# Performance work log

Hardware: AMD Instinct MI355X
Metric: run time of the kernel (lower is better)

Reference implementation:

```python
import math
import jax, jax.numpy as jnp
import numpy as np

# ---- hard-coded constants from the source module ----
T_H = 1.5; M = 60; DT = T_H / M; SQDT = math.sqrt(DT)
ALPHA = 0.8; RHO = 0.3; SQ1MR2 = math.sqrt(1.0 - RHO * RHO)
GAMMA = 5.0; KAPPA_Y = 1.2; LB_W = 1e-3
R = 0.02; SIGMA = 0.2; SIGMA_Y = 0.3; THETA_Y = 0.0; PI_CAP = 2.0
RPTS = 128       # sub_batch (one accumulation iteration)
REPEATS = 128    # total repeats == sub_batch -> single loop pass
N_PTS = 32       # number of eval states
HID = 64


def setup_inputs():
    key = jax.random.key(0)
    ks = jax.random.split(key, 8)
    W = 0.8 + 0.4 * jax.random.uniform(ks[0], (N_PTS, 1), jnp.float32)   # W0_range
    Y = -1.0 + 2.0 * jax.random.uniform(ks[1], (N_PTS, 1), jnp.float32)  # Y0_range
    TmT = jnp.full((N_PTS, 1), T_H, jnp.float32)
    B = RPTS * N_PTS
    # [sim(+/-), draw(z1/z2), step, path, 1] -- fresh noise per antithetic branch, as in torch
    noise = jax.random.normal(ks[2], (2, 2, M, B, 1), jnp.float32)
    w1 = 0.1 * jax.random.normal(ks[3], (3, HID), jnp.float32)
    b1 = jnp.zeros((HID,), jnp.float32)
    w2 = 0.1 * jax.random.normal(ks[4], (HID, HID), jnp.float32)
    b2 = jnp.zeros((HID,), jnp.float32)
    w3 = 0.1 * jax.random.normal(ks[5], (HID, 1), jnp.float32)
    b3 = jnp.zeros((1,), jnp.float32)
    return {"W": W, "TmT": TmT, "Y": Y, "noise": noise,
            "w1": w1, "b1": b1, "w2": w2, "b2": b2, "w3": w3, "b3": b3}


def _policy(params, W, TmT, Y):
    w1, b1, w2, b2, w3, b3 = params
    x = jnp.concatenate([W, TmT, Y], axis=-1)          # [B,3]
    h = jnp.tanh(x @ w1 + b1)
    h = jnp.tanh(h @ w2 + b2)
    return h @ w3 + b3                                 # [B,1]


def _simulate(params, W0, Y0, z1, z2, anti):
    """60-step Euler-Maruyama; returns CRRA utility U(W_T), shape [B,1]."""
    logW = jnp.log(jnp.clip(W0, LB_W, None))
    TmT0 = jnp.full_like(W0, T_H)

    def step(carry, zs):
        logW, Y, TmT = carry
        z1s, z2s = zs
        pi = _policy(params, jnp.exp(logW), TmT, Y)
        zW = anti * z1s
        zY = anti * (RHO * z1s + SQ1MR2 * z2s)
        drift = R + pi * (SIGMA * ALPHA * Y)
        var = (pi * SIGMA) ** 2
        logW = logW + (drift - 0.5 * var) * DT + pi * SIGMA * SQDT * zW
        Y = Y + KAPPA_Y * (THETA_Y - Y) * DT + SIGMA_Y * SQDT * zY
        logW = jnp.log(jnp.clip(jnp.exp(logW), LB_W, None))
        return (logW, Y, TmT - DT), None

    (logW, _, _), _ = jax.lax.scan(step, (logW, Y0, TmT0), (z1, z2))
    W_T = jnp.exp(logW)
    return W_T ** (1.0 - GAMMA) / (1.0 - GAMMA)        # gamma != 1


def reference(W, TmT, Y, noise, w1, b1, w2, b2, w3, b3):
    params = (w1, b1, w2, b2, w3, b3)
    n = W.shape[0]
    Wd = jax.lax.stop_gradient(W)   # forward detaches W, Y
    Yd = jax.lax.stop_gradient(Y)
    W0 = jnp.tile(Wd, (RPTS, 1))    # [B,1]
    Y0 = jnp.tile(Yd, (RPTS, 1))
    z1p, z2p = noise[0, 0], noise[0, 1]
    z1m, z2m = noise[1, 0], noise[1, 1]

    def f(W0_, Y0_):
        U = 0.5 * (_simulate(params, W0_, Y0_, z1p, z2p, 1.0)
                   + _simulate(params, W0_, Y0_, z1m, z2m, -1.0))
        # U_avg.sum() as in torch: mean over rpts, sum over eval points
        return jnp.sum(jnp.mean(U.reshape(RPTS, n), axis=0))

    lam_full = jax.grad(f, 0)(W0, Y0)                  # [B,1]

    def g(W0_, Y0_):
        # lam.view(rpts,n,1).mean(0).sum() == sum(lam_full)/rpts
        return jnp.sum(jax.grad(f, 0)(W0_, Y0_)) / RPTS

    dW_full, dY_full = jax.grad(g, (0, 1))(W0, Y0)     # [B,1] each

    inv = 1.0 / REPEATS   # faithful to source accumulation scaling
    lam = lam_full.reshape(RPTS, n, 1).mean(0) * inv
    dlamW = dW_full.reshape(RPTS, n, 1).mean(0) * inv
    dlamY = dY_full.reshape(RPTS, n, 1).mean(0) * inv

    # project_pmp
    mu_minus_r = SIGMA * (ALPHA * Yd)
    coeff = -1.0 / (Wd * dlamW + 1e-8)
    myo = coeff * (lam * (mu_minus_r / SIGMA ** 2))
    hedge = coeff * (SIGMA * RHO * SIGMA_Y * dlamY / SIGMA ** 2)
    return jnp.clip(myo + hedge, -PI_CAP, PI_CAP)      # [n,1]
```

## Files before the change

kernel.cpp:

```cpp
#include <hip/hip_runtime.h>
#include <math.h>

#define HID    64
#define MSTEPS 60
#define NPTS   32
#define RPTSC  128
#define BTOT   (RPTSC*NPTS)
#define NSIM   (2*BTOT)
#define NWAVE  (NSIM/2)

#define C_DT     0.025f
#define C_SQDT   0.15811388300841897f
#define C_ALPHA  0.8f
#define C_RHO    0.3f
#define C_SQ1MR2 0.9539392014169456f
#define C_KAPPA  1.2f
#define C_R      0.02f
#define C_SIGMA  0.2f
#define C_SIGY   0.3f
#define C_LBW    1e-3f
#define C_LOGLBW -6.907755279f
#define C_2L2E   2.8853900817779268f

#define WAVE_LDS 3584
#define A_ROW    144
#define OFF_DV   2304
#define OFF_DA   3328

typedef _Float16 half8 __attribute__((ext_vector_type(8)));
typedef float    f32x4 __attribute__((ext_vector_type(4)));
typedef _Float16 h2    __attribute__((ext_vector_type(2)));

__device__ __forceinline__ float rlanef(float v, int l) {
    return __int_as_float(__builtin_amdgcn_readlane(__float_as_int(v), l));
}
template <int OFF>
__device__ __forceinline__ float swz(float v) {
    return __int_as_float(__builtin_amdgcn_ds_swizzle(__float_as_int(v), OFF));
}
__device__ __forceinline__ f32x4 MFMA(half8 a, half8 b, f32x4 c) {
    return __builtin_amdgcn_mfma_f32_16x16x32_f16(a, b, c, 0, 0, 0);
}
__device__ __forceinline__ int pk16(float a, float b) {
    return __builtin_bit_cast(int, __builtin_amdgcn_cvt_pkrtz(a, b));
}
__device__ __forceinline__ h2 pk2(float a, float b) {
    return __builtin_bit_cast(h2, __builtin_amdgcn_cvt_pkrtz(a, b));
}
__device__ __forceinline__ h2 permh(unsigned s0, unsigned s1, unsigned sel) {
    return __builtin_bit_cast(h2, __builtin_amdgcn_perm(s0, s1, sel));
}
__device__ __forceinline__ float tanh_fast(float xs) {
    return 1.0f - 2.0f * __builtin_amdgcn_rcpf(__builtin_amdgcn_exp2f(xs) + 1.0f);
}

__global__ __launch_bounds__(256, 4) void sim_kernel(
    const float* __restrict__ noise,
    const float* __restrict__ w1, const float* __restrict__ b1,
    const float* __restrict__ w2, const float* __restrict__ b2,
    const float* __restrict__ w3, const float* __restrict__ b3,
    const float* __restrict__ Wp, const float* __restrict__ Yp,
    float* __restrict__ sd)
{
    __shared__ __align__(16) char smem[4 * WAVE_LDS];
    const int lane = threadIdx.x & 63;
    const int quad = lane >> 4;
    const int mrow = lane & 15;
    const int par  = lane >> 5;
    char* wb = smem + (threadIdx.x >> 6) * WAVE_LDS;

    const int w = __builtin_amdgcn_readfirstlane(
        (int)((blockIdx.x * blockDim.x + threadIdx.x) >> 6));
    const int simb = w >> 11;
    const int pg   = 2*(w & 2047) + par;
    const int i    = pg & (NPTS - 1);

    const float cW  = w1[lane];
    const float cT  = w1[HID + lane];
    const float cYw = w1[2*HID + lane];
    const float b1k = b1[lane];
    const float b2k = b2[lane];
    const float b3v = b3[0];
    const float cW_s  = cW  * C_2L2E;
    const float cT_s  = cT  * C_2L2E;
    const float cYw_s = cYw * C_2L2E;
    const float b1_s  = b1k * C_2L2E;
    const float b2_s  = b2k * C_2L2E;
    const h2 cWh  = pk2(cW, cW);
    const h2 cYwh = pk2(cYw, cYw);
    const h2 cW2m = pk2(-2.0f*cW*cW,  -2.0f*cW*cW);
    const h2 cWYm = pk2(-2.0f*cW*cYw, -2.0f*cW*cYw);
    const h2 hone = {(_Float16)1.0f,  (_Float16)1.0f};
    const h2 m2h  = {(_Float16)-2.0f, (_Float16)-2.0f};

    half8 B00, B01, B02, B03, B10, B11, B12, B13, W30, W31;
    {
        half8 h;
        #define LOADB(dst, q, t) \
            { for (int j = 0; j < 8; ++j) \
                h[j] = (_Float16)w2[((q)*32 + quad*8 + j)*HID + (t)*16 + mrow]; \
              dst = h; }
        LOADB(B00, 0, 0) LOADB(B01, 0, 1) LOADB(B02, 0, 2) LOADB(B03, 0, 3)
        LOADB(B10, 1, 0) LOADB(B11, 1, 1) LOADB(B12, 1, 2) LOADB(B13, 1, 3)
        #undef LOADB
        for (int j = 0; j < 8; ++j) h[j] = (_Float16)w3[0*32 + quad*8 + j];
        W30 = h;
        for (int j = 0; j < 8; ++j) h[j] = (_Float16)w3[1*32 + quad*8 + j];
        W31 = h;
    }

    for (int off = lane*4; off < 16*A_ROW; off += 256)
        *(float*)(wb + off) = 0.0f;

    _Float16* swp = (_Float16*)(wb + lane*2);
    char* arp0 = wb + mrow*A_ROW + quad*16;

    const float* zp1 = noise + (size_t)(simb*2 + 0) * MSTEPS * BTOT + pg;
    const float* zp2 = noise + (size_t)(simb*2 + 1) * MSTEPS * BTOT + pg;

    const float anti = simb ? -1.0f : 1.0f;
    const float ksa  = C_SIGMA * C_ALPHA;
    const float ks2  = C_SIGMA * C_SIGMA;
    const float ksn  = anti * C_SIGMA * C_SQDT;
    const float kFy  = ksa * C_DT;
    const float ksd  = ks2 * C_DT;
    const float kv   = 0.5f * ks2 * C_DT;
    const float kRdt = C_R * C_DT;
    const float ky1  = anti * C_SIGY * C_SQDT * C_RHO;
    const float ky2  = anti * C_SIGY * C_SQDT * C_SQ1MR2;
    const float cYfac = 1.0f - C_KAPPA * C_DT;

    const float W0 = Wp[i];
    float L   = __logf(fmaxf(W0, C_LBW));
    float W   = __expf(L);
    float Yv  = Yp[i];
    float tmt = 1.5f;
    float gW  = 1.0f / W0;
    float hWW = -gW * gW;
    float gY  = 0.0f, hWY = 0.0f;
    float cYt = 1.0f;

    #pragma unroll 1
    for (int m = 0; m < MSTEPS; ++m) {
        asm volatile("" : "+v"(B00), "+v"(B01), "+v"(B02), "+v"(B03),
                          "+v"(B10), "+v"(B11), "+v"(B12), "+v"(B13),
                          "+v"(W30), "+v"(W31));

        const float z1 = zp1[(size_t)m * BTOT];
        const float z2 = zp2[(size_t)m * BTOT];

        const float Wb0 = rlanef(W, 0),  Wb1 = rlanef(W, 32);
        const float Yb0 = rlanef(Yv, 0), Yb1 = rlanef(Yv, 32);

        const float base1s = fmaf(tmt, cT_s, b1_s);
        {
            const float t10 = tanh_fast(fmaf(Wb0, cW_s, fmaf(Yb0, cYw_s, base1s)));
            const float t11 = tanh_fast(fmaf(Wb1, cW_s, fmaf(Yb1, cYw_s, base1s)));
            const h2 tp  = pk2(t10, t11);
            const h2 dpp = hone - tp * tp;
            const h2 ddq = tp * dpp;
            const h2 r1 = dpp * cWh;
            const h2 r2 = dpp * cYwh;
            const h2 r3 = ddq * cW2m;
            const h2 r4 = ddq * cWYm;
            swp[0*72] = tp.x;  swp[8*72]  = tp.y;
            swp[1*72] = r1.x;  swp[9*72]  = r1.y;
            swp[2*72] = r2.x;  swp[10*72] = r2.y;
            swp[3*72] = r3.x;  swp[11*72] = r3.y;
            swp[4*72] = r4.x;  swp[12*72] = r4.y;
        }

        half8 af0 = __builtin_bit_cast(half8, *(const f32x4*)arp0);
        half8 af1 = __builtin_bit_cast(half8, *(const f32x4*)(arp0 + 64));

        f32x4 acc[4];
        const f32x4 zz = {0.f, 0.f, 0.f, 0.f};
        acc[0] = MFMA(af1, B10, MFMA(af0, B00, zz));
        acc[1] = MFMA(af1, B11, MFMA(af0, B01, zz));
        acc[2] = MFMA(af1, B12, MFMA(af0, B02, zz));
        acc[3] = MFMA(af1, B13, MFMA(af0, B03, zz));

        {
            const int p = quad >> 1;
            if (!(quad & 1)) {
                #pragma unroll
                for (int t = 0; t < 4; ++t) {
                    int2 v;
                    v.x = pk16(acc[t].x, acc[t].y);
                    v.y = pk16(acc[t].z, acc[t].w);
                    *(int2*)(wb + OFF_DV + ((t*16 + mrow) << 4) + (p << 3)) = v;
                }
            } else {
                #pragma unroll
                for (int t = 0; t < 4; ++t)
                    *(_Float16*)(wb + OFF_DA + ((t*16 + mrow) << 2) + (p << 1)) =
                        (_Float16)acc[t].x;
            }
        }

        const f32x4 dvv = *(const f32x4*)(wb + OFF_DV + lane*16);
        const h2 awyp   = *(const h2*)(wb + OFF_DA + lane*4);
        {
            const unsigned q0 = __builtin_bit_cast(unsigned, dvv.x);
            const unsigned q1 = __builtin_bit_cast(unsigned, dvv.y);
            const unsigned q2 = __builtin_bit_cast(unsigned, dvv.z);
            const unsigned q3 = __builtin_bit_cast(unsigned, dvv.w);
            const h2 a0p  = permh(q2, q0, 0x05040100);
            const h2 aWp  = permh(q2, q0, 0x07060302);
            const h2 aYp  = permh(q3, q1, 0x05040100);
            const h2 aWWp = permh(q3, q1, 0x07060302);

            const float t20 = tanh_fast(fmaf((float)a0p.x, C_2L2E, b2_s));
            const float t21 = tanh_fast(fmaf((float)a0p.y, C_2L2E, b2_s));
            const h2 t2p = pk2(t20, t21);
            const h2 d2p = hone - t2p * t2p;
            const h2 qp  = (m2h * (t2p * d2p)) * aWp;
            const h2 s1 = d2p * aWp;
            const h2 s2 = d2p * aYp;
            const h2 s3 = qp * aWp + d2p * aWWp;
            const h2 s4 = qp * aYp + d2p * awyp;
            swp[0*72] = t2p.x; swp[8*72]  = t2p.y;
            swp[1*72] = s1.x;  swp[9*72]  = s1.y;
            swp[2*72] = s2.x;  swp[10*72] = s2.y;
            swp[3*72] = s3.x;  swp[11*72] = s3.y;
            swp[4*72] = s4.x;  swp[12*72] = s4.y;
        }

        half8 bf0 = __builtin_bit_cast(half8, *(const f32x4*)arp0);
        half8 bf1 = __builtin_bit_cast(half8, *(const f32x4*)(arp0 + 64));
        f32x4 acc4 = MFMA(bf1, W31, MFMA(bf0, W30, zz));

        const float pi  = swz<0x0000>(acc4.x) + b3v;
        const float pW  = swz<0x0000>(acc4.y);
        const float pY  = swz<0x0000>(acc4.z);
        const float pWW = swz<0x0000>(acc4.w);
        const float pWY = swz<0x0200>(acc4.x);

        const float Sn    = ksn * z1;
        const float say   = ksa * Yv;
        const float G     = fmaf(-ks2, pi, say);
        const float GdtSn = fmaf(G, C_DT, Sn);

        const float w2v  = W * W;
        const float piL  = pW * W;
        const float piLL = fmaf(pWW, w2v, piL);
        const float piY  = pY;
        const float piLY = pWY * W;

        const float pi2  = pi * pi;
        const float Lnew = fmaf(pi, fmaf(say, C_DT, Sn),
                                fmaf(-kv, pi2, L + kRdt));

        const float F_L  = fmaf(piL, GdtSn, 1.0f);
        const float F_Y  = fmaf(piY, GdtSn, kFy * pi);
        const float piL2 = piL * piL;
        const float F_LL = fmaf(piLL, GdtSn, -(ksd * piL2));
        const float F_LY = fmaf(piLY, GdtSn, piL * fmaf(-ksd, piY, kFy));

        const float gW2  = gW * gW;
        const float hWWn = fmaf(F_LL, gW2, F_L * hWW);
        const float hWYn = fmaf(F_LL, gW * gY,
                                fmaf(F_LY, gW * cYt, F_L * hWY));
        const float gWn  = F_L * gW;
        const float gYn  = fmaf(F_Y, cYt, F_L * gY);

        Yv  = fmaf(ky2, z2, fmaf(ky1, z1, cYfac * Yv));
        cYt *= cYfac;

        const float We   = __expf(Lnew);
        const bool  clip = (We < C_LBW);
        L   = clip ? C_LOGLBW : Lnew;
        W   = clip ? C_LBW    : We;
        gW  = clip ? 0.0f : gWn;
        gY  = clip ? 0.0f : gYn;
        hWW = clip ? 0.0f : hWWn;
        hWY = clip ? 0.0f : hWYn;
        tmt -= C_DT;
    }

    const float E   = __expf(-4.0f * L);
    const float d1  = E * gW;
    const float d2v = fmaf(-4.0f * E, gW * gW, E * hWW);
    const float d3v = fmaf(-4.0f * E, gW * gY, E * hWY);

    if ((lane & 31) == 0) {
        const int branch = simb * BTOT + pg;
        sd[         branch] = 0.5f * d1;
        sd[  NSIM + branch] = 0.5f * d2v;
        sd[2*NSIM + branch] = 0.5f * d3v;
    }
}

__global__ __launch_bounds__(512) void proj_kernel(
    const float* __restrict__ sd,
    const float* __restrict__ Wp,
    const float* __restrict__ Yp,
    float* __restrict__ out)
{
    __shared__ float red[3 * 512];
    const int tid = threadIdx.x;
    const int i = tid & 31;
    const int c = tid >> 5;
    float lam = 0.f, dW = 0.f, dY = 0.f;
    #pragma unroll 4
    for (int jj = 0; jj < 16; ++jj) {
        const int idx = i + ((jj*16 + c) << 5);
        lam += sd[idx];
        dW  += sd[NSIM + idx];
        dY  += sd[2*NSIM + idx];
    }
    red[tid] = lam; red[512 + tid] = dW; red[1024 + tid] = dY;
    __syncthreads();
    if (tid < NPTS) {
        float l = 0.f, w = 0.f, y = 0.f;
        #pragma unroll
        for (int c2 = 0; c2 < 16; ++c2) {
            l += red[c2*32 + i];
            w += red[512 + c2*32 + i];
            y += red[1024 + c2*32 + i];
        }
        l *= (1.0f / 2097152.0f);
        w *= (1.0f / 268435456.0f);
        y *= (1.0f / 268435456.0f);
        const float Wv = Wp[i], Yv = Yp[i];
        const float mmr   = C_SIGMA * (C_ALPHA * Yv);
        const float sig2  = C_SIGMA * C_SIGMA;
        const float coeff = -1.0f / (Wv * w + 1e-8f);
        const float myo   = coeff * (l * (mmr / sig2));
        const float hedge = coeff * (C_SIGMA * C_RHO * C_SIGY * y / sig2);
        float v = myo + hedge;
        v = fminf(fmaxf(v, -2.0f), 2.0f);
        out[i] = v;
    }
}

extern "C" void kernel_launch(void* const* d_in, const int* in_sizes, int n_in,
                              void* d_out, int out_size, void* d_ws, size_t ws_size,
                              hipStream_t stream) {
    const float* Wp    = (const float*)d_in[0];
    const float* Yp    = (const float*)d_in[2];
    const float* noise = (const float*)d_in[3];
    const float* w1    = (const float*)d_in[4];
    const float* b1    = (const float*)d_in[5];
    const float* w2    = (const float*)d_in[6];
    const float* b2    = (const float*)d_in[7];
    const float* w3    = (const float*)d_in[8];
    const float* b3    = (const float*)d_in[9];
    float* out = (float*)d_out;
    float* sd  = (float*)d_ws;

    hipLaunchKernelGGL(sim_kernel, dim3(NWAVE/4), dim3(256), 0, stream,
                       noise, w1, b1, w2, b2, w3, b3, Wp, Yp, sd);
    hipLaunchKernelGGL(proj_kernel, dim3(1), dim3(512), 0, stream, sd, Wp, Yp, out);
}
```

Baseline: 163.0 us.

## Replace second LDS round trip and output MFMA with in-register layer-2 epilogue and DPP reduction

New measurement: 171.1 us. 5.0% more time.

```diff
diff --git a/kernel.cpp b/kernel.cpp
--- a/kernel.cpp
+++ b/kernel.cpp
@@ -22,10 +22,8 @@
 #define C_LOGLBW -6.907755279f
 #define C_2L2E   2.8853900817779268f
 
-#define WAVE_LDS 3584
+#define WAVE_LDS 2304
 #define A_ROW    144
-#define OFF_DV   2304
-#define OFF_DA   3328
 
 typedef _Float16 half8 __attribute__((ext_vector_type(8)));
 typedef float    f32x4 __attribute__((ext_vector_type(4)));
@@ -41,17 +39,23 @@
 __device__ __forceinline__ f32x4 MFMA(half8 a, half8 b, f32x4 c) {
     return __builtin_amdgcn_mfma_f32_16x16x32_f16(a, b, c, 0, 0, 0);
 }
-__device__ __forceinline__ int pk16(float a, float b) {
-    return __builtin_bit_cast(int, __builtin_amdgcn_cvt_pkrtz(a, b));
-}
 __device__ __forceinline__ h2 pk2(float a, float b) {
     return __builtin_bit_cast(h2, __builtin_amdgcn_cvt_pkrtz(a, b));
 }
-__device__ __forceinline__ h2 permh(unsigned s0, unsigned s1, unsigned sel) {
-    return __builtin_bit_cast(h2, __builtin_amdgcn_perm(s0, s1, sel));
-}
 __device__ __forceinline__ float tanh_fast(float xs) {
     return 1.0f - 2.0f * __builtin_amdgcn_rcpf(__builtin_amdgcn_exp2f(xs) + 1.0f);
+}
+template <int CTRL>
+__device__ __forceinline__ float dppadd(float v) {
+    return v + __int_as_float(__builtin_amdgcn_update_dpp(
+        0, __float_as_int(v), CTRL, 0xf, 0xf, false));
+}
+__device__ __forceinline__ float red64(float v) {
+    v = dppadd<0x121>(v);
+    v = dppadd<0x122>(v);
+    v = dppadd<0x124>(v);
+    v = dppadd<0x128>(v);
+    return v + swz<0x401F>(v);
 }
 
 __global__ __launch_bounds__(256, 4) void sim_kernel(
@@ -91,9 +95,13 @@
     const h2 cW2m = pk2(-2.0f*cW*cW,  -2.0f*cW*cW);
     const h2 cWYm = pk2(-2.0f*cW*cYw, -2.0f*cW*cYw);
     const h2 hone = {(_Float16)1.0f,  (_Float16)1.0f};
-    const h2 m2h  = {(_Float16)-2.0f, (_Float16)-2.0f};
-
-    half8 B00, B01, B02, B03, B10, B11, B12, B13, W30, W31;
+
+    const float w3q0 = (quad & 1) ? 0.0f : w3[ 0 + mrow];
+    const float w3q1 = (quad & 1) ? 0.0f : w3[16 + mrow];
+    const float w3q2 = (quad & 1) ? 0.0f : w3[32 + mrow];
+    const float w3q3 = (quad & 1) ? 0.0f : w3[48 + mrow];
+
+    half8 B00, B01, B02, B03, B10, B11, B12, B13;
     {
         half8 h;
         #define LOADB(dst, q, t) \
@@ -103,10 +111,6 @@
         LOADB(B00, 0, 0) LOADB(B01, 0, 1) LOADB(B02, 0, 2) LOADB(B03, 0, 3)
         LOADB(B10, 1, 0) LOADB(B11, 1, 1) LOADB(B12, 1, 2) LOADB(B13, 1, 3)
         #undef LOADB
-        for (int j = 0; j < 8; ++j) h[j] = (_Float16)w3[0*32 + quad*8 + j];
-        W30 = h;
-        for (int j = 0; j < 8; ++j) h[j] = (_Float16)w3[1*32 + quad*8 + j];
-        W31 = h;
     }
 
     for (int off = lane*4; off < 16*A_ROW; off += 256)
@@ -140,14 +144,18 @@
     float gY  = 0.0f, hWY = 0.0f;
     float cYt = 1.0f;
 
+    float z1c = zp1[0];
+    float z2c = zp2[0];
+
     #pragma unroll 1
     for (int m = 0; m < MSTEPS; ++m) {
         asm volatile("" : "+v"(B00), "+v"(B01), "+v"(B02), "+v"(B03),
-                          "+v"(B10), "+v"(B11), "+v"(B12), "+v"(B13),
-                          "+v"(W30), "+v"(W31));
-
-        const float z1 = zp1[(size_t)m * BTOT];
-        const float z2 = zp2[(size_t)m * BTOT];
+                          "+v"(B10), "+v"(B11), "+v"(B12), "+v"(B13));
+
+        const float z1 = z1c, z2 = z2c;
+        const int mn = (m + 1 < MSTEPS) ? m + 1 : m;
+        z1c = zp1[(size_t)mn * BTOT];
+        z2c = zp2[(size_t)mn * BTOT];
 
         const float Wb0 = rlanef(W, 0),  Wb1 = rlanef(W, 32);
         const float Yb0 = rlanef(Yv, 0), Yb1 = rlanef(Yv, 32);
@@ -180,61 +188,40 @@
         acc[2] = MFMA(af1, B12, MFMA(af0, B02, zz));
         acc[3] = MFMA(af1, B13, MFMA(af0, B03, zz));
 
-        {
-            const int p = quad >> 1;
-            if (!(quad & 1)) {
-                #pragma unroll
-                for (int t = 0; t < 4; ++t) {
-                    int2 v;
-                    v.x = pk16(acc[t].x, acc[t].y);
-                    v.y = pk16(acc[t].z, acc[t].w);
-                    *(int2*)(wb + OFF_DV + ((t*16 + mrow) << 4) + (p << 3)) = v;
-                }
-            } else {
-                #pragma unroll
-                for (int t = 0; t < 4; ++t)
-                    *(_Float16*)(wb + OFF_DA + ((t*16 + mrow) << 2) + (p << 1)) =
-                        (_Float16)acc[t].x;
-            }
+        float awy[4];
+        awy[0] = swz<0x401F>(acc[0].x);
+        awy[1] = swz<0x401F>(acc[1].x);
+        awy[2] = swz<0x401F>(acc[2].x);
+        awy[3] = swz<0x401F>(acc[3].x);
+        const float w3qa[4] = {w3q0, w3q1, w3q2, w3q3};
+
+        float p0 = 0.f, p1 = 0.f, p2 = 0.f, p3 = 0.f, p4 = 0.f;
+        #pragma unroll
+        for (int t = 0; t < 4; ++t) {
+            const float a0  = acc[t].x, aW = acc[t].y;
+            const float aY  = acc[t].z, aWW = acc[t].w;
+            const float aWY = awy[t];
+            const float t2  = tanh_fast(fmaf(a0, C_2L2E, b2_s));
+            const float d2  = fmaf(-t2, t2, 1.0f);
+            const float td  = t2 * d2;
+            const float q   = -2.0f * (td * aW);
+            const float s1  = d2 * aW;
+            const float s2  = d2 * aY;
+            const float s3  = fmaf(q, aW, d2 * aWW);
+            const float s4  = fmaf(q, aY, d2 * aWY);
+            const float w3t = w3qa[t];
+            p0 = fmaf(t2, w3t, p0);
+            p1 = fmaf(s1, w3t, p1);
+            p2 = fmaf(s2, w3t, p2);
+            p3 = fmaf(s3, w3t, p3);
+            p4 = fmaf(s4, w3t, p4);
         }
 
-        const f32x4 dvv = *(const f32x4*)(wb + OFF_DV + lane*16);
-        const h2 awyp   = *(const h2*)(wb + OFF_DA + lane*4);
-        {
-            const unsigned q0 = __builtin_bit_cast(unsigned, dvv.x);
-            const unsigned q1 = __builtin_bit_cast(unsigned, dvv.y);
-            const unsigned q2 = __builtin_bit_cast(unsigned, dvv.z);
-            const unsigned q3 = __builtin_bit_cast(unsigned, dvv.w);
-            const h2 a0p  = permh(q2, q0, 0x05040100);
-            const h2 aWp  = permh(q2, q0, 0x07060302);
-            const h2 aYp  = permh(q3, q1, 0x05040100);
-            const h2 aWWp = permh(q3, q1, 0x07060302);
-
-            const float t20 = tanh_fast(fmaf((float)a0p.x, C_2L2E, b2_s));
-            const float t21 = tanh_fast(fmaf((float)a0p.y, C_2L2E, b2_s));
-            const h2 t2p = pk2(t20, t21);
-            const h2 d2p = hone - t2p * t2p;
-            const h2 qp  = (m2h * (t2p * d2p)) * aWp;
-            const h2 s1 = d2p * aWp;
-            const h2 s2 = d2p * aYp;
-            const h2 s3 = qp * aWp + d2p * aWWp;
-            const h2 s4 = qp * aYp + d2p * awyp;
-            swp[0*72] = t2p.x; swp[8*72]  = t2p.y;
-            swp[1*72] = s1.x;  swp[9*72]  = s1.y;
-            swp[2*72] = s2.x;  swp[10*72] = s2.y;
-            swp[3*72] = s3.x;  swp[11*72] = s3.y;
-            swp[4*72] = s4.x;  swp[12*72] = s4.y;
-        }
-
-        half8 bf0 = __builtin_bit_cast(half8, *(const f32x4*)arp0);
-        half8 bf1 = __builtin_bit_cast(half8, *(const f32x4*)(arp0 + 64));
-        f32x4 acc4 = MFMA(bf1, W31, MFMA(bf0, W30, zz));
-
-        const float pi  = swz<0x0000>(acc4.x) + b3v;
-        const float pW  = swz<0x0000>(acc4.y);
-        const float pY  = swz<0x0000>(acc4.z);
-        const float pWW = swz<0x0000>(acc4.w);
-        const float pWY = swz<0x0200>(acc4.x);
+        const float pi  = red64(p0) + b3v;
+        const float pW  = red64(p1);
+        const float pY  = red64(p2);
+        const float pWW = red64(p3);
+        const float pWY = red64(p4);
 
         const float Sn    = ksn * z1;
         const float say   = ksa * Yv;
```

## Interleave two independent path pairs per wave to hide MFMA and LDS latency

Applied to the files above, without the earlier changes.

Measured after the change: 171.8 us. 5.4% more time.

```diff
diff --git a/kernel.cpp b/kernel.cpp
--- a/kernel.cpp
+++ b/kernel.cpp
@@ -7,7 +7,8 @@
 #define RPTSC  128
 #define BTOT   (RPTSC*NPTS)
 #define NSIM   (2*BTOT)
-#define NWAVE  (NSIM/2)
+#define NWAVE  2048
+#define NBLK   (NWAVE/4)
 
 #define C_DT     0.025f
 #define C_SQDT   0.15811388300841897f
@@ -22,7 +23,7 @@
 #define C_LOGLBW -6.907755279f
 #define C_2L2E   2.8853900817779268f
 
-#define WAVE_LDS 3584
+#define PAIR_LDS 3584
 #define A_ROW    144
 #define OFF_DV   2304
 #define OFF_DA   3328
@@ -54,7 +55,77 @@
     return 1.0f - 2.0f * __builtin_amdgcn_rcpf(__builtin_amdgcn_exp2f(xs) + 1.0f);
 }
 
-__global__ __launch_bounds__(256, 4) void sim_kernel(
+__device__ __forceinline__ void l1_jets(
+    _Float16* swp, float bW0, float bW1, float bY0, float bY1,
+    float base1s, float cW_s, float cYw_s,
+    h2 cWh, h2 cYwh, h2 cW2m, h2 cWYm)
+{
+    const h2 hone = {(_Float16)1.0f, (_Float16)1.0f};
+    const float t10 = tanh_fast(fmaf(bW0, cW_s, fmaf(bY0, cYw_s, base1s)));
+    const float t11 = tanh_fast(fmaf(bW1, cW_s, fmaf(bY1, cYw_s, base1s)));
+    const h2 tp  = pk2(t10, t11);
+    const h2 dpp = hone - tp * tp;
+    const h2 ddq = tp * dpp;
+    const h2 r1 = dpp * cWh;
+    const h2 r2 = dpp * cYwh;
+    const h2 r3 = ddq * cW2m;
+    const h2 r4 = ddq * cWYm;
+    swp[0*72] = tp.x;  swp[8*72]  = tp.y;
+    swp[1*72] = r1.x;  swp[9*72]  = r1.y;
+    swp[2*72] = r2.x;  swp[10*72] = r2.y;
+    swp[3*72] = r3.x;  swp[11*72] = r3.y;
+    swp[4*72] = r4.x;  swp[12*72] = r4.y;
+}
+
+__device__ __forceinline__ void dxpose(char* wb, const f32x4* acc, int quad, int mrow)
+{
+    const int p = quad >> 1;
+    if (!(quad & 1)) {
+        #pragma unroll
+        for (int t = 0; t < 4; ++t) {
+            int2 v;
+            v.x = pk16(acc[t].x, acc[t].y);
+            v.y = pk16(acc[t].z, acc[t].w);
+            *(int2*)(wb + OFF_DV + ((t*16 + mrow) << 4) + (p << 3)) = v;
+        }
+    } else {
+        #pragma unroll
+        for (int t = 0; t < 4; ++t)
+            *(_Float16*)(wb + OFF_DA + ((t*16 + mrow) << 2) + (p << 1)) =
+                (_Float16)acc[t].x;
+    }
+}
+
+__device__ __forceinline__ void l2_jets(_Float16* swp, f32x4 dvv, h2 awyp, float b2_s)
+{
+    const h2 hone = {(_Float16)1.0f,  (_Float16)1.0f};
+    const h2 m2h  = {(_Float16)-2.0f, (_Float16)-2.0f};
+    const unsigned q0 = __builtin_bit_cast(unsigned, dvv.x);
+    const unsigned q1 = __builtin_bit_cast(unsigned, dvv.y);
+    const unsigned q2 = __builtin_bit_cast(unsigned, dvv.z);
+    const unsigned q3 = __builtin_bit_cast(unsigned, dvv.w);
+    const h2 a0p  = permh(q2, q0, 0x05040100);
+    const h2 aWp  = permh(q2, q0, 0x07060302);
+    const h2 aYp  = permh(q3, q1, 0x05040100);
+    const h2 aWWp = permh(q3, q1, 0x07060302);
+
+    const float t20 = tanh_fast(fmaf((float)a0p.x, C_2L2E, b2_s));
+    const float t21 = tanh_fast(fmaf((float)a0p.y, C_2L2E, b2_s));
+    const h2 t2p = pk2(t20, t21);
+    const h2 d2p = hone - t2p * t2p;
+    const h2 qp  = (m2h * (t2p * d2p)) * aWp;
+    const h2 s1 = d2p * aWp;
+    const h2 s2 = d2p * aYp;
+    const h2 s3 = qp * aWp + d2p * aWWp;
+    const h2 s4 = qp * aYp + d2p * awyp;
+    swp[0*72] = t2p.x; swp[8*72]  = t2p.y;
+    swp[1*72] = s1.x;  swp[9*72]  = s1.y;
+    swp[2*72] = s2.x;  swp[10*72] = s2.y;
+    swp[3*72] = s3.x;  swp[11*72] = s3.y;
+    swp[4*72] = s4.x;  swp[12*72] = s4.y;
+}
+
+__global__ __launch_bounds__(256, 2) void sim_kernel(
     const float* __restrict__ noise,
     const float* __restrict__ w1, const float* __restrict__ b1,
     const float* __restrict__ w2, const float* __restrict__ b2,
@@ -62,18 +133,21 @@
     const float* __restrict__ Wp, const float* __restrict__ Yp,
     float* __restrict__ sd)
 {
-    __shared__ __align__(16) char smem[4 * WAVE_LDS];
+    __shared__ __align__(16) char smem[4 * 2 * PAIR_LDS];
     const int lane = threadIdx.x & 63;
     const int quad = lane >> 4;
     const int mrow = lane & 15;
     const int par  = lane >> 5;
-    char* wb = smem + (threadIdx.x >> 6) * WAVE_LDS;
+    char* wbA = smem + (threadIdx.x >> 6) * (2 * PAIR_LDS);
+    char* wbB = wbA + PAIR_LDS;
 
     const int w = __builtin_amdgcn_readfirstlane(
         (int)((blockIdx.x * blockDim.x + threadIdx.x) >> 6));
-    const int simb = w >> 11;
-    const int pg   = 2*(w & 2047) + par;
-    const int i    = pg & (NPTS - 1);
+    const int simb = w >> 10;
+    const int pga  = 4*(w & 1023) + par;
+    const int pgb  = pga + 2;
+    const int ia   = pga & (NPTS - 1);
+    const int ib   = pgb & (NPTS - 1);
 
     const float cW  = w1[lane];
     const float cT  = w1[HID + lane];
@@ -90,8 +164,6 @@
     const h2 cYwh = pk2(cYw, cYw);
     const h2 cW2m = pk2(-2.0f*cW*cW,  -2.0f*cW*cW);
     const h2 cWYm = pk2(-2.0f*cW*cYw, -2.0f*cW*cYw);
-    const h2 hone = {(_Float16)1.0f,  (_Float16)1.0f};
-    const h2 m2h  = {(_Float16)-2.0f, (_Float16)-2.0f};
 
     half8 B00, B01, B02, B03, B10, B11, B12, B13, W30, W31;
     {
@@ -109,14 +181,18 @@
         W31 = h;
     }
 
-    for (int off = lane*4; off < 16*A_ROW; off += 256)
-        *(float*)(wb + off) = 0.0f;
-
-    _Float16* swp = (_Float16*)(wb + lane*2);
-    char* arp0 = wb + mrow*A_ROW + quad*16;
-
-    const float* zp1 = noise + (size_t)(simb*2 + 0) * MSTEPS * BTOT + pg;
-    const float* zp2 = noise + (size_t)(simb*2 + 1) * MSTEPS * BTOT + pg;
+    for (int off = lane*4; off < 16*A_ROW; off += 256) {
+        *(float*)(wbA + off) = 0.0f;
+        *(float*)(wbB + off) = 0.0f;
+    }
+
+    _Float16* swpA = (_Float16*)(wbA + lane*2);
+    _Float16* swpB = (_Float16*)(wbB + lane*2);
+    char* arpA = wbA + mrow*A_ROW + quad*16;
+    char* arpB = wbB + mrow*A_ROW + quad*16;
+
+    const float* zp1 = noise + (size_t)(simb*2 + 0) * MSTEPS * BTOT + pga;
+    const float* zp2 = noise + (size_t)(simb*2 + 1) * MSTEPS * BTOT + pga;
 
     const float anti = simb ? -1.0f : 1.0f;
     const float ksa  = C_SIGMA * C_ALPHA;
@@ -130,112 +206,22 @@
     const float ky2  = anti * C_SIGY * C_SQDT * C_SQ1MR2;
     const float cYfac = 1.0f - C_KAPPA * C_DT;
 
-    const float W0 = Wp[i];
-    float L   = __logf(fmaxf(W0, C_LBW));
-    float W   = __expf(L);
-    float Yv  = Yp[i];
+    const float W0a = Wp[ia], W0b = Wp[ib];
+    float La = __logf(fmaxf(W0a, C_LBW)), Lb = __logf(fmaxf(W0b, C_LBW));
+    float Wa = __expf(La),                Wb = __expf(Lb);
+    float Ya = Yp[ia],                    Yb = Yp[ib];
+    float gWa = 1.0f / W0a,               gWb = 1.0f / W0b;
+    float hWWa = -gWa * gWa,              hWWb = -gWb * gWb;
+    float gYa = 0.0f, hWYa = 0.0f,        gYb = 0.0f, hWYb = 0.0f;
     float tmt = 1.5f;
-    float gW  = 1.0f / W0;
-    float hWW = -gW * gW;
-    float gY  = 0.0f, hWY = 0.0f;
     float cYt = 1.0f;
 
-    #pragma unroll 1
-    for (int m = 0; m < MSTEPS; ++m) {
-        asm volatile("" : "+v"(B00), "+v"(B01), "+v"(B02), "+v"(B03),
-                          "+v"(B10), "+v"(B11), "+v"(B12), "+v"(B13),
-                          "+v"(W30), "+v"(W31));
-
-        const float z1 = zp1[(size_t)m * BTOT];
-        const float z2 = zp2[(size_t)m * BTOT];
-
-        const float Wb0 = rlanef(W, 0),  Wb1 = rlanef(W, 32);
-        const float Yb0 = rlanef(Yv, 0), Yb1 = rlanef(Yv, 32);
-
-        const float base1s = fmaf(tmt, cT_s, b1_s);
-        {
-            const float t10 = tanh_fast(fmaf(Wb0, cW_s, fmaf(Yb0, cYw_s, base1s)));
-            const float t11 = tanh_fast(fmaf(Wb1, cW_s, fmaf(Yb1, cYw_s, base1s)));
-            const h2 tp  = pk2(t10, t11);
-            const h2 dpp = hone - tp * tp;
-            const h2 ddq = tp * dpp;
-            const h2 r1 = dpp * cWh;
-            const h2 r2 = dpp * cYwh;
-            const h2 r3 = ddq * cW2m;
-            const h2 r4 = ddq * cWYm;
-            swp[0*72] = tp.x;  swp[8*72]  = tp.y;
-            swp[1*72] = r1.x;  swp[9*72]  = r1.y;
-            swp[2*72] = r2.x;  swp[10*72] = r2.y;
-            swp[3*72] = r3.x;  swp[11*72] = r3.y;
-            swp[4*72] = r4.x;  swp[12*72] = r4.y;
-        }
-
-        half8 af0 = __builtin_bit_cast(half8, *(const f32x4*)arp0);
-        half8 af1 = __builtin_bit_cast(half8, *(const f32x4*)(arp0 + 64));
-
-        f32x4 acc[4];
-        const f32x4 zz = {0.f, 0.f, 0.f, 0.f};
-        acc[0] = MFMA(af1, B10, MFMA(af0, B00, zz));
-        acc[1] = MFMA(af1, B11, MFMA(af0, B01, zz));
-        acc[2] = MFMA(af1, B12, MFMA(af0, B02, zz));
-        acc[3] = MFMA(af1, B13, MFMA(af0, B03, zz));
-
-        {
-            const int p = quad >> 1;
-            if (!(quad & 1)) {
-                #pragma unroll
-                for (int t = 0; t < 4; ++t) {
-                    int2 v;
-                    v.x = pk16(acc[t].x, acc[t].y);
-                    v.y = pk16(acc[t].z, acc[t].w);
-                    *(int2*)(wb + OFF_DV + ((t*16 + mrow) << 4) + (p << 3)) = v;
-                }
-            } else {
-                #pragma unroll
-                for (int t = 0; t < 4; ++t)
-                    *(_Float16*)(wb + OFF_DA + ((t*16 + mrow) << 2) + (p << 1)) =
-                        (_Float16)acc[t].x;
-            }
-        }
-
-        const f32x4 dvv = *(const f32x4*)(wb + OFF_DV + lane*16);
-        const h2 awyp   = *(const h2*)(wb + OFF_DA + lane*4);
-        {
-            const unsigned q0 = __builtin_bit_cast(unsigned, dvv.x);
-            const unsigned q1 = __builtin_bit_cast(unsigned, dvv.y);
-            const unsigned q2 = __builtin_bit_cast(unsigned, dvv.z);
-            const unsigned q3 = __builtin_bit_cast(unsigned, dvv.w);
-            const h2 a0p  = permh(q2, q0, 0x05040100);
-            const h2 aWp  = permh(q2, q0, 0x07060302);
-            const h2 aYp  = permh(q3, q1, 0x05040100);
-            const h2 aWWp = permh(q3, q1, 0x07060302);
-
-            const float t20 = tanh_fast(fmaf((float)a0p.x, C_2L2E, b2_s));
-            const float t21 = tanh_fast(fmaf((float)a0p.y, C_2L2E, b2_s));
-            const h2 t2p = pk2(t20, t21);
-            const h2 d2p = hone - t2p * t2p;
-            const h2 qp  = (m2h * (t2p * d2p)) * aWp;
-            const h2 s1 = d2p * aWp;
-            const h2 s2 = d2p * aYp;
-            const h2 s3 = qp * aWp + d2p * aWWp;
-            const h2 s4 = qp * aYp + d2p * awyp;
-            swp[0*72] = t2p.x; swp[8*72]  = t2p.y;
-            swp[1*72] = s1.x;  swp[9*72]  = s1.y;
-            swp[2*72] = s2.x;  swp[10*72] = s2.y;
-            swp[3*72] = s3.x;  swp[11*72] = s3.y;
-            swp[4*72] = s4.x;  swp[12*72] = s4.y;
-        }
-
-        half8 bf0 = __builtin_bit_cast(half8, *(const f32x4*)arp0);
-        half8 bf1 = __builtin_bit_cast(half8, *(const f32x4*)(arp0 + 64));
-        f32x4 acc4 = MFMA(bf1, W31, MFMA(bf0, W30, zz));
-
-        const float pi  = swz<0x0000>(acc4.x) + b3v;
-        const float pW  = swz<0x0000>(acc4.y);
-        const float pY  = swz<0x0000>(acc4.z);
-        const float pWW = swz<0x0000>(acc4.w);
-        const float pWY = swz<0x0200>(acc4.x);
-
+    float z1ca = zp1[0], z2ca = zp2[0];
+    float z1cb = zp1[2], z2cb = zp2[2];
+
+    auto dyn = [&](float& L, float& W, float& Yv, float& gW, float& gY,
+                   float& hWW, float& hWY, float z1, float z2,
+                   float pi, float pW, float pY, float pWW, float pWY) {
         const float Sn    = ksn * z1;
         const float say   = ksa * Yv;
         const float G     = fmaf(-ks2, pi, say);
@@ -264,8 +250,7 @@
         const float gWn  = F_L * gW;
         const float gYn  = fmaf(F_Y, cYt, F_L * gY);
 
-        Yv  = fmaf(ky2, z2, fmaf(ky1, z1, cYfac * Yv));
-        cYt *= cYfac;
+        Yv = fmaf(ky2, z2, fmaf(ky1, z1, cYfac * Yv));
 
         const float We   = __expf(Lnew);
         const bool  clip = (We < C_LBW);
@@ -275,19 +260,98 @@
         gY  = clip ? 0.0f : gYn;
         hWW = clip ? 0.0f : hWWn;
         hWY = clip ? 0.0f : hWYn;
+    };
+
+    #pragma unroll 1
+    for (int m = 0; m < MSTEPS; ++m) {
+        asm volatile("" : "+v"(B00), "+v"(B01), "+v"(B02), "+v"(B03),
+                          "+v"(B10), "+v"(B11), "+v"(B12), "+v"(B13),
+                          "+v"(W30), "+v"(W31));
+
+        const float z1a = z1ca, z2a = z2ca, z1b = z1cb, z2b = z2cb;
+        const int mn = (m + 1 < MSTEPS) ? m + 1 : m;
+        z1ca = zp1[(size_t)mn * BTOT];     z2ca = zp2[(size_t)mn * BTOT];
+        z1cb = zp1[(size_t)mn * BTOT + 2]; z2cb = zp2[(size_t)mn * BTOT + 2];
+
+        const float bWa0 = rlanef(Wa, 0), bWa1 = rlanef(Wa, 32);
+        const float bYa0 = rlanef(Ya, 0), bYa1 = rlanef(Ya, 32);
+        const float bWb0 = rlanef(Wb, 0), bWb1 = rlanef(Wb, 32);
+        const float bYb0 = rlanef(Yb, 0), bYb1 = rlanef(Yb, 32);
+
+        const float base1s = fmaf(tmt, cT_s, b1_s);
+        l1_jets(swpA, bWa0, bWa1, bYa0, bYa1, base1s, cW_s, cYw_s,
+                cWh, cYwh, cW2m, cWYm);
+        l1_jets(swpB, bWb0, bWb1, bYb0, bYb1, base1s, cW_s, cYw_s,
+                cWh, cYwh, cW2m, cWYm);
+
+        half8 afA0 = __builtin_bit_cast(half8, *(const f32x4*)arpA);
+        half8 afA1 = __builtin_bit_cast(half8, *(const f32x4*)(arpA + 64));
+        half8 afB0 = __builtin_bit_cast(half8, *(const f32x4*)arpB);
+        half8 afB1 = __builtin_bit_cast(half8, *(const f32x4*)(arpB + 64));
+
+        f32x4 accA[4], accB[4];
+        const f32x4 zz = {0.f, 0.f, 0.f, 0.f};
+        accA[0] = MFMA(afA1, B10, MFMA(afA0, B00, zz));
+        accB[0] = MFMA(afB1, B10, MFMA(afB0, B00, zz));
+        accA[1] = MFMA(afA1, B11, MFMA(afA0, B01, zz));
+        accB[1] = MFMA(afB1, B11, MFMA(afB0, B01, zz));
+        accA[2] = MFMA(afA1, B12, MFMA(afA0, B02, zz));
+        accB[2] = MFMA(afB1, B12, MFMA(afB0, B02, zz));
+        accA[3] = MFMA(afA1, B13, MFMA(afA0, B03, zz));
+        accB[3] = MFMA(afB1, B13, MFMA(afB0, B03, zz));
+
+        dxpose(wbA, accA, quad, mrow);
+        dxpose(wbB, accB, quad, mrow);
+
+        const f32x4 dvA = *(const f32x4*)(wbA + OFF_DV + (lane << 4));
+        const h2   awA  = *(const h2*)  (wbA + OFF_DA + (lane << 2));
+        const f32x4 dvB = *(const f32x4*)(wbB + OFF_DV + (lane << 4));
+        const h2   awB  = *(const h2*)  (wbB + OFF_DA + (lane << 2));
+        l2_jets(swpA, dvA, awA, b2_s);
+        l2_jets(swpB, dvB, awB, b2_s);
+
+        half8 bfA0 = __builtin_bit_cast(half8, *(const f32x4*)arpA);
+        half8 bfA1 = __builtin_bit_cast(half8, *(const f32x4*)(arpA + 64));
+        half8 bfB0 = __builtin_bit_cast(half8, *(const f32x4*)arpB);
+        half8 bfB1 = __builtin_bit_cast(half8, *(const f32x4*)(arpB + 64));
+        f32x4 acc4A = MFMA(bfA1, W31, MFMA(bfA0, W30, zz));
+        f32x4 acc4B = MFMA(bfB1, W31, MFMA(bfB0, W30, zz));
+
+        const float piA  = swz<0x0000>(acc4A.x) + b3v;
+        const float pWA  = swz<0x0000>(acc4A.y);
+        const float pYA  = swz<0x0000>(acc4A.z);
+        const float pWWA = swz<0x0000>(acc4A.w);
+        const float pWYA = swz<0x0200>(acc4A.x);
+        const float piB  = swz<0x0000>(acc4B.x) + b3v;
+        const float pWB  = swz<0x0000>(acc4B.y);
+        const float pYB  = swz<0x0000>(acc4B.z);
+        const float pWWB = swz<0x0000>(acc4B.w);
+        const float pWYB = swz<0x0200>(acc4B.x);
+
+        dyn(La, Wa, Ya, gWa, gYa, hWWa, hWYa, z1a, z2a,
+            piA, pWA, pYA, pWWA, pWYA);
+        dyn(Lb, Wb, Yb, gWb, gYb, hWWb, hWYb, z1b, z2b,
+            piB, pWB, pYB, pWWB, pWYB);
+
+        cYt *= cYfac;
         tmt -= C_DT;
     }
 
-    const float E   = __expf(-4.0f * L);
-    const float d1  = E * gW;
-    const float d2v = fmaf(-4.0f * E, gW * gW, E * hWW);
-    const float d3v = fmaf(-4.0f * E, gW * gY, E * hWY);
-
     if ((lane & 31) == 0) {
-        const int branch = simb * BTOT + pg;
-        sd[         branch] = 0.5f * d1;
-        sd[  NSIM + branch] = 0.5f * d2v;
-        sd[2*NSIM + branch] = 0.5f * d3v;
+        const int brA = simb * BTOT + pga;
+        const int brB = brA + 2;
+        {
+            const float E = __expf(-4.0f * La);
+            sd[         brA] = 0.5f * (E * gWa);
+            sd[  NSIM + brA] = 0.5f * fmaf(-4.0f * E, gWa * gWa, E * hWWa);
+            sd[2*NSIM + brA] = 0.5f * fmaf(-4.0f * E, gWa * gYa, E * hWYa);
+        }
+        {
+            const float E = __expf(-4.0f * Lb);
+            sd[         brB] = 0.5f * (E * gWb);
+            sd[  NSIM + brB] = 0.5f * fmaf(-4.0f * E, gWb * gWb, E * hWWb);
+            sd[2*NSIM + brB] = 0.5f * fmaf(-4.0f * E, gWb * gYb, E * hWYb);
+        }
     }
 }
 
@@ -349,7 +413,7 @@
     float* out = (float*)d_out;
     float* sd  = (float*)d_ws;
 
-    hipLaunchKernelGGL(sim_kernel, dim3(NWAVE/4), dim3(256), 0, stream,
+    hipLaunchKernelGGL(sim_kernel, dim3(NBLK), dim3(256), 0, stream,
                        noise, w1, b1, w2, b2, w3, b3, Wp, Yp, sd);
     hipLaunchKernelGGL(proj_kernel, dim3(1), dim3(512), 0, stream, sd, Wp, Yp, out);
 }
```

## Prefetch next-step noise, pack DA LDS stores, replace swizzle broadcasts with readlane

Applied to the files above, without the earlier changes.

Result: no change. 163.1 us (+0.0%).

```diff
diff --git a/kernel.cpp b/kernel.cpp
--- a/kernel.cpp
+++ b/kernel.cpp
@@ -8,6 +8,7 @@
 #define BTOT   (RPTSC*NPTS)
 #define NSIM   (2*BTOT)
 #define NWAVE  (NSIM/2)
+#define NBLK   (NWAVE/4)
 
 #define C_DT     0.025f
 #define C_SQDT   0.15811388300841897f
@@ -33,10 +34,6 @@
 
 __device__ __forceinline__ float rlanef(float v, int l) {
     return __int_as_float(__builtin_amdgcn_readlane(__float_as_int(v), l));
-}
-template <int OFF>
-__device__ __forceinline__ float swz(float v) {
-    return __int_as_float(__builtin_amdgcn_ds_swizzle(__float_as_int(v), OFF));
 }
 __device__ __forceinline__ f32x4 MFMA(half8 a, half8 b, f32x4 c) {
     return __builtin_amdgcn_mfma_f32_16x16x32_f16(a, b, c, 0, 0, 0);
@@ -67,6 +64,7 @@
     const int quad = lane >> 4;
     const int mrow = lane & 15;
     const int par  = lane >> 5;
+    const bool phi = (par != 0);
     char* wb = smem + (threadIdx.x >> 6) * WAVE_LDS;
 
     const int w = __builtin_amdgcn_readfirstlane(
@@ -92,6 +90,7 @@
     const h2 cWYm = pk2(-2.0f*cW*cYw, -2.0f*cW*cYw);
     const h2 hone = {(_Float16)1.0f,  (_Float16)1.0f};
     const h2 m2h  = {(_Float16)-2.0f, (_Float16)-2.0f};
+    const unsigned daSel = (quad & 1) ? 0x07060302u : 0x05040100u;
 
     half8 B00, B01, B02, B03, B10, B11, B12, B13, W30, W31;
     {
@@ -114,6 +113,8 @@
 
     _Float16* swp = (_Float16*)(wb + lane*2);
     char* arp0 = wb + mrow*A_ROW + quad*16;
+    char* daw = wb + OFF_DA + ((quad >> 1) << 7) + (mrow << 2);
+    char* dar = wb + OFF_DA + ((lane >> 5) << 6) + (mrow << 2);
 
     const float* zp1 = noise + (size_t)(simb*2 + 0) * MSTEPS * BTOT + pg;
     const float* zp2 = noise + (size_t)(simb*2 + 1) * MSTEPS * BTOT + pg;
@@ -140,14 +141,19 @@
     float gY  = 0.0f, hWY = 0.0f;
     float cYt = 1.0f;
 
+    float z1c = zp1[0];
+    float z2c = zp2[0];
+
     #pragma unroll 1
     for (int m = 0; m < MSTEPS; ++m) {
         asm volatile("" : "+v"(B00), "+v"(B01), "+v"(B02), "+v"(B03),
                           "+v"(B10), "+v"(B11), "+v"(B12), "+v"(B13),
                           "+v"(W30), "+v"(W31));
 
-        const float z1 = zp1[(size_t)m * BTOT];
-        const float z2 = zp2[(size_t)m * BTOT];
+        const float z1 = z1c, z2 = z2c;
+        const int mn = (m + 1 < MSTEPS) ? m + 1 : m;
+        z1c = zp1[(size_t)mn * BTOT];
+        z2c = zp2[(size_t)mn * BTOT];
 
         const float Wb0 = rlanef(W, 0),  Wb1 = rlanef(W, 32);
         const float Yb0 = rlanef(Yv, 0), Yb1 = rlanef(Yv, 32);
@@ -191,15 +197,16 @@
                     *(int2*)(wb + OFF_DV + ((t*16 + mrow) << 4) + (p << 3)) = v;
                 }
             } else {
-                #pragma unroll
-                for (int t = 0; t < 4; ++t)
-                    *(_Float16*)(wb + OFF_DA + ((t*16 + mrow) << 2) + (p << 1)) =
-                        (_Float16)acc[t].x;
+                const int d0 = pk16(acc[0].x, acc[1].x);
+                const int d1 = pk16(acc[2].x, acc[3].x);
+                *(int*)daw        = d0;
+                *(int*)(daw + 64) = d1;
             }
         }
 
         const f32x4 dvv = *(const f32x4*)(wb + OFF_DV + lane*16);
-        const h2 awyp   = *(const h2*)(wb + OFF_DA + lane*4);
+        const int da_lo = *(const int*)dar;
+        const int da_hi = *(const int*)(dar + 128);
         {
             const unsigned q0 = __builtin_bit_cast(unsigned, dvv.x);
             const unsigned q1 = __builtin_bit_cast(unsigned, dvv.y);
@@ -209,6 +216,7 @@
             const h2 aWp  = permh(q2, q0, 0x07060302);
             const h2 aYp  = permh(q3, q1, 0x05040100);
             const h2 aWWp = permh(q3, q1, 0x07060302);
+            const h2 awyp = permh((unsigned)da_hi, (unsigned)da_lo, daSel);
 
             const float t20 = tanh_fast(fmaf((float)a0p.x, C_2L2E, b2_s));
             const float t21 = tanh_fast(fmaf((float)a0p.y, C_2L2E, b2_s));
@@ -230,11 +238,16 @@
         half8 bf1 = __builtin_bit_cast(half8, *(const f32x4*)(arp0 + 64));
         f32x4 acc4 = MFMA(bf1, W31, MFMA(bf0, W30, zz));
 
-        const float pi  = swz<0x0000>(acc4.x) + b3v;
-        const float pW  = swz<0x0000>(acc4.y);
-        const float pY  = swz<0x0000>(acc4.z);
-        const float pWW = swz<0x0000>(acc4.w);
-        const float pWY = swz<0x0200>(acc4.x);
+        const float pi0  = rlanef(acc4.x,  0), pi1  = rlanef(acc4.x, 32);
+        const float pW0  = rlanef(acc4.y,  0), pW1  = rlanef(acc4.y, 32);
+        const float pY0  = rlanef(acc4.z,  0), pY1  = rlanef(acc4.z, 32);
+        const float pWW0 = rlanef(acc4.w,  0), pWW1 = rlanef(acc4.w, 32);
+        const float pWY0 = rlanef(acc4.x, 16), pWY1 = rlanef(acc4.x, 48);
+        const float pi  = (phi ? pi1  : pi0) + b3v;
+        const float pW  = phi ? pW1  : pW0;
+        const float pY  = phi ? pY1  : pY0;
+        const float pWW = phi ? pWW1 : pWW0;
+        const float pWY = phi ? pWY1 : pWY0;
 
         const float Sn    = ksn * z1;
         const float say   = ksa * Yv;
@@ -349,7 +362,7 @@
     float* out = (float*)d_out;
     float* sd  = (float*)d_ws;
 
-    hipLaunchKernelGGL(sim_kernel, dim3(NWAVE/4), dim3(256), 0, stream,
+    hipLaunchKernelGGL(sim_kernel, dim3(NBLK), dim3(256), 0, stream,
                        noise, w1, b1, w2, b2, w3, b3, Wp, Yp, sd);
     hipLaunchKernelGGL(proj_kernel, dim3(1), dim3(512), 0, stream, sd, Wp, Yp, out);
 }
```
